# Performance work log

Measured on AMD Instinct MI355X. Metric: run time of the kernel, lower is better.

## Reference

```python
import jax, jax.numpy as jnp
import numpy as np

B, T, D_MODEL, HEADS = 2, 2048, 1024, 16
D_HEAD = D_MODEL // HEADS


def setup_inputs() -> dict:
    key = jax.random.key(0)
    ks = jax.random.split(key, 9)
    s = 1.0 / np.sqrt(D_HEAD)
    return {
        "x": jax.random.normal(ks[0], (B, T, D_MODEL), dtype=jnp.float32),
        "Wq": jax.random.normal(ks[1], (D_HEAD, D_HEAD), dtype=jnp.float32) * s,
        "bq": jax.random.normal(ks[2], (D_HEAD,), dtype=jnp.float32) * 0.01,
        "Wk": jax.random.normal(ks[3], (D_HEAD, D_HEAD), dtype=jnp.float32) * s,
        "bk": jax.random.normal(ks[4], (D_HEAD,), dtype=jnp.float32) * 0.01,
        "Wv": jax.random.normal(ks[5], (D_HEAD, D_HEAD), dtype=jnp.float32) * s,
        "bv": jax.random.normal(ks[6], (D_HEAD,), dtype=jnp.float32) * 0.01,
        "Wp": jax.random.normal(ks[7], (D_MODEL, D_MODEL), dtype=jnp.float32) * (1.0 / np.sqrt(D_MODEL)),
        "bp": jax.random.normal(ks[8], (D_MODEL,), dtype=jnp.float32) * 0.01,
    }


def reference(x, Wq, bq, Wk, bk, Wv, bv, Wp, bp):
    b, t, c = x.shape
    xh = x.reshape(b, t, HEADS, D_HEAD)  # [B,T,H,dh]
    # per-head linear projections (weights shared across heads), nn.Linear: y = x @ W.T + b
    q = jnp.einsum('bthd,ed->bhte', xh, Wq) + bq  # [B,H,T,dh]
    k = jnp.einsum('bthd,ed->bhte', xh, Wk) + bk
    v = jnp.einsum('bthd,ed->bhte', xh, Wv) + bv
    # NOTE: original scales by sqrt(C) = sqrt(d_model), not sqrt(d_head)
    scale = 1.0 / jnp.sqrt(jnp.float32(c))
    att = jnp.einsum('bhqd,bhkd->bhqk', q, k) * scale  # [B,H,T,T]
    att = jax.nn.softmax(att, axis=-1)
    out = jnp.einsum('bhqk,bhkd->bhqd', att, v)  # [B,H,T,dh]
    out = out.transpose(0, 2, 1, 3).reshape(b, t, c)  # [B,T,C]
    out = out @ Wp.T + bp
    return out
```

## Files before the change

### kernel.cpp

```cpp
#include <hip/hip_runtime.h>
#include <hip/hip_bf16.h>

#define B_ 2
#define T_ 2048
#define DM_ 1024
#define H_ 16
#define DH_ 64
#define QSCALE 0.045084220027780106f

typedef unsigned short u16;
typedef unsigned int u32;
typedef __attribute__((ext_vector_type(2))) unsigned int u32x2;
typedef __attribute__((ext_vector_type(4))) unsigned int u32x4;
typedef __attribute__((ext_vector_type(4))) float f32x4v;
typedef __attribute__((ext_vector_type(8))) short bf16x8;
typedef __attribute__((ext_vector_type(4))) float f32x4;
typedef __attribute__((ext_vector_type(16))) float f32x16;

__device__ __forceinline__ u16 f2bf(float f) {
    u32 u = __float_as_uint(f);
    return (u16)((u + 0x7FFF + ((u >> 16) & 1)) >> 16);
}
__device__ __forceinline__ float bf2f(u16 h) {
    return __uint_as_float(((u32)h) << 16);
}
__device__ __forceinline__ float exp2_fast(float x) {
    float r;
    asm("v_exp_f32 %0, %1" : "=v"(r) : "v"(x));
    return r;
}
__device__ __forceinline__ u32 cvtpk_bf16(float lo, float hi) {
    u32 r;
    asm("v_cvt_pk_bf16_f32 %0, %1, %2" : "=v"(r) : "v"(lo), "v"(hi));
    return r;
}

__device__ __forceinline__ const bf16x8* frag_at(const u16* base, int row, int c16) {
    return (const bf16x8*)((const char*)base + row * 128 + ((c16 ^ (row & 7)) << 4));
}

__global__ __launch_bounds__(256) void wsplit_all(
    const float* __restrict__ Wq, const float* __restrict__ Wk,
    const float* __restrict__ Wv, const float* __restrict__ Wp,
    u16* __restrict__ W6, u16* __restrict__ Wh, u16* __restrict__ Wl)
{
    const int i = blockIdx.x * 256 + threadIdx.x;
    if (i < DM_ * DM_) {
        const float w = Wp[i];
        const u16 hi = f2bf(w);
        Wh[i] = hi;
        Wl[i] = f2bf(w - bf2f(hi));
    } else {
        const int j = i - DM_ * DM_;
        const int mat = j >> 12, idx = j & 4095;
        const float w = (mat == 0) ? Wq[idx] : (mat == 1) ? Wk[idx] : Wv[idx];
        const u16 hi = f2bf(w);
        W6[(mat * 2) * 4096 + idx] = hi;
        W6[(mat * 2 + 1) * 4096 + idx] = f2bf(w - bf2f(hi));
    }
}

__global__ __launch_bounds__(256) void qkv_mfma(
    const float* __restrict__ x,
    const float* __restrict__ bq, const float* __restrict__ bk,
    const float* __restrict__ bv, const u16* __restrict__ W6,
    u16* __restrict__ Q, u16* __restrict__ K, u16* __restrict__ VT)
{
    __shared__ u16 Ws[6 * 4096];

    const int tid = threadIdx.x;
    const int wid = tid >> 6;
    const int lane = tid & 63;
    const int li = lane & 15, g = lane >> 4;

    const int bh = blockIdx.x >> 4;
    const int t0 = (blockIdx.x & 15) * 128;
    const int b = bh >> 4, h = bh & 15;
    const int tw0 = t0 + wid * 32;

    #pragma unroll
    for (int j = 0; j < 12; ++j) {
        const int gi = j * 256 + tid;
        const int tile = gi >> 9;
        const int t16 = gi & 511;
        const int r = t16 >> 3, c16 = t16 & 7;
        const int c16s = c16 ^ (r & 7);
        __builtin_amdgcn_global_load_lds(
            (const __attribute__((address_space(1))) u32*)((const char*)W6 + tile * 8192 + r * 128 + (c16s << 4)),
            (__attribute__((address_space(3))) u32*)((char*)Ws + gi * 16),
            16, 0, 0);
    }

    const float* xb = x + ((size_t)b * T_) * DM_ + h * 64;
    f32x4v xr[2][2][2];
    #pragma unroll
    for (int mt = 0; mt < 2; ++mt)
        #pragma unroll
        for (int kt = 0; kt < 2; ++kt) {
            const float* p = xb + (size_t)(tw0 + 16 * mt + li) * DM_ + kt * 32 + g * 8;
            xr[mt][kt][0] = *(const f32x4v*)p;
            xr[mt][kt][1] = *(const f32x4v*)(p + 4);
        }

    float bq_r[4], bk_r[4], bv_r[4][4];
    #pragma unroll
    for (int nt = 0; nt < 4; ++nt) { bq_r[nt] = bq[16 * nt + li]; bk_r[nt] = bk[16 * nt + li]; }
    #pragma unroll
    for (int vd = 0; vd < 4; ++vd)
        #pragma unroll
        for (int rg = 0; rg < 4; ++rg) bv_r[vd][rg] = bv[16 * vd + 4 * g + rg];

    __syncthreads();

    bf16x8 xhf[2][2], xlf[2][2];
    #pragma unroll
    for (int mt = 0; mt < 2; ++mt)
        #pragma unroll
        for (int kt = 0; kt < 2; ++kt) {
            u32 hw[4], lw[4];
            #pragma unroll
            for (int q2 = 0; q2 < 2; ++q2) {
                const f32x4v v = xr[mt][kt][q2];
                const u32 p0 = cvtpk_bf16(v[0], v[1]);
                const u32 p1 = cvtpk_bf16(v[2], v[3]);
                const float l0 = v[0] - __uint_as_float(p0 << 16);
                const float l1 = v[1] - __uint_as_float(p0 & 0xFFFF0000u);
                const float l2 = v[2] - __uint_as_float(p1 << 16);
                const float l3 = v[3] - __uint_as_float(p1 & 0xFFFF0000u);
                hw[q2 * 2] = p0; hw[q2 * 2 + 1] = p1;
                lw[q2 * 2] = cvtpk_bf16(l0, l1);
                lw[q2 * 2 + 1] = cvtpk_bf16(l2, l3);
            }
            xhf[mt][kt] = *(const bf16x8*)hw;
            xlf[mt][kt] = *(const bf16x8*)lw;
        }

    const u16* Wqh = Ws;
    const u16* Wql = Ws + 4096;
    const u16* Wkh = Ws + 8192;
    const u16* Wkl = Ws + 12288;
    const u16* Wvh = Ws + 16384;
    const u16* Wvl = Ws + 20480;

    const size_t qk_base = ((size_t)bh * T_) * DH_;

    {
        f32x4 acc[2][4];
        #pragma unroll
        for (int mt = 0; mt < 2; ++mt)
            #pragma unroll
            for (int nt = 0; nt < 4; ++nt) acc[mt][nt] = (f32x4){0.f, 0.f, 0.f, 0.f};
        #pragma unroll
        for (int nt = 0; nt < 4; ++nt)
            #pragma unroll
            for (int kt = 0; kt < 2; ++kt) {
                const bf16x8 wh = *frag_at(Wqh, 16 * nt + li, 4 * kt + g);
                const bf16x8 wl = *frag_at(Wql, 16 * nt + li, 4 * kt + g);
                #pragma unroll
                for (int mt = 0; mt < 2; ++mt) {
                    acc[mt][nt] = __builtin_amdgcn_mfma_f32_16x16x32_bf16(xhf[mt][kt], wh, acc[mt][nt], 0, 0, 0);
                    acc[mt][nt] = __builtin_amdgcn_mfma_f32_16x16x32_bf16(xlf[mt][kt], wh, acc[mt][nt], 0, 0, 0);
                    acc[mt][nt] = __builtin_amdgcn_mfma_f32_16x16x32_bf16(xhf[mt][kt], wl, acc[mt][nt], 0, 0, 0);
                }
            }
        #pragma unroll
        for (int mt = 0; mt < 2; ++mt)
            #pragma unroll
            for (int rg = 0; rg < 4; ++rg) {
                const int t = tw0 + 16 * mt + 4 * g + rg;
                #pragma unroll
                for (int nt = 0; nt < 4; ++nt)
                    Q[qk_base + (size_t)t * DH_ + 16 * nt + li] =
                        f2bf((acc[mt][nt][rg] + bq_r[nt]) * QSCALE);
            }
    }

    {
        f32x4 acc[2][4];
        #pragma unroll
        for (int mt = 0; mt < 2; ++mt)
            #pragma unroll
            for (int nt = 0; nt < 4; ++nt) acc[mt][nt] = (f32x4){0.f, 0.f, 0.f, 0.f};
        #pragma unroll
        for (int nt = 0; nt < 4; ++nt)
            #pragma unroll
            for (int kt = 0; kt < 2; ++kt) {
                const bf16x8 wh = *frag_at(Wkh, 16 * nt + li, 4 * kt + g);
                const bf16x8 wl = *frag_at(Wkl, 16 * nt + li, 4 * kt + g);
                #pragma unroll
                for (int mt = 0; mt < 2; ++mt) {
                    acc[mt][nt] = __builtin_amdgcn_mfma_f32_16x16x32_bf16(xhf[mt][kt], wh, acc[mt][nt], 0, 0, 0);
                    acc[mt][nt] = __builtin_amdgcn_mfma_f32_16x16x32_bf16(xlf[mt][kt], wh, acc[mt][nt], 0, 0, 0);
                    acc[mt][nt] = __builtin_amdgcn_mfma_f32_16x16x32_bf16(xhf[mt][kt], wl, acc[mt][nt], 0, 0, 0);
                }
            }
        #pragma unroll
        for (int mt = 0; mt < 2; ++mt)
            #pragma unroll
            for (int rg = 0; rg < 4; ++rg) {
                const int t = tw0 + 16 * mt + 4 * g + rg;
                #pragma unroll
                for (int nt = 0; nt < 4; ++nt)
                    K[qk_base + (size_t)t * DH_ + 16 * nt + li] =
                        f2bf(acc[mt][nt][rg] + bk_r[nt]);
            }
    }

    {
        f32x4 acc[4][2];
        #pragma unroll
        for (int vd = 0; vd < 4; ++vd)
            #pragma unroll
            for (int tc = 0; tc < 2; ++tc) acc[vd][tc] = (f32x4){0.f, 0.f, 0.f, 0.f};
        #pragma unroll
        for (int vd = 0; vd < 4; ++vd)
            #pragma unroll
            for (int kt = 0; kt < 2; ++kt) {
                const bf16x8 ah = *frag_at(Wvh, 16 * vd + li, 4 * kt + g);
                const bf16x8 al = *frag_at(Wvl, 16 * vd + li, 4 * kt + g);
                #pragma unroll
                for (int tc = 0; tc < 2; ++tc) {
                    acc[vd][tc] = __builtin_amdgcn_mfma_f32_16x16x32_bf16(ah, xhf[tc][kt], acc[vd][tc], 0, 0, 0);
                    acc[vd][tc] = __builtin_amdgcn_mfma_f32_16x16x32_bf16(al, xhf[tc][kt], acc[vd][tc], 0, 0, 0);
                    acc[vd][tc] = __builtin_amdgcn_mfma_f32_16x16x32_bf16(ah, xlf[tc][kt], acc[vd][tc], 0, 0, 0);
                }
            }
        u16* VTb = VT + (size_t)bh * DH_ * T_;
        #pragma unroll
        for (int vd = 0; vd < 4; ++vd)
            #pragma unroll
            for (int rg = 0; rg < 4; ++rg) {
                const int d = 16 * vd + 4 * g + rg;
                #pragma unroll
                for (int tc = 0; tc < 2; ++tc)
                    VTb[(size_t)d * T_ + tw0 + 16 * tc + li] =
                        f2bf(acc[vd][tc][rg] + bv_r[vd][rg]);
            }
    }
}

__global__ __launch_bounds__(256) void attn_mfma(
    const u16* __restrict__ Q, const u16* __restrict__ K,
    const u16* __restrict__ VT, u16* __restrict__ Ah, u16* __restrict__ Al)
{
    __shared__ char smem[65536];

    const int tid = threadIdx.x;
    const int wid = tid >> 6;
    const int lane = tid & 63;
    const int l = lane & 31, h = lane >> 5;
    const int flat = blockIdx.x;
    const int bh = (flat & 7) + ((flat >> 7) << 3);
    const int qx = (flat >> 3) & 15;
    const int q0 = qx * 128 + wid * 32;

    const size_t bhoff = (size_t)bh * T_ * DH_;

    bf16x8 qf[4];
    {
        const u16* Qp = Q + bhoff + (size_t)(q0 + l) * DH_ + 8 * h;
        #pragma unroll
        for (int kt = 0; kt < 4; ++kt)
            qf[kt] = *(const bf16x8*)(Qp + 16 * kt);
    }

    f32x16 o0 = {}, o1 = {};
    f32x16 sA, sB, sC, sD;
    float l_part = 0.f;

    const char* ldsR[4];
    #pragma unroll
    for (int j = 0; j < 4; ++j)
        ldsR[j] = smem + l * 128 + ((((2 * j + h) ^ (l & 7))) << 4);

    const int sl_r = lane >> 3;
    const int sl_c = (lane & 7) ^ sl_r;
    const char* kgp = (const char*)(K + bhoff) + (32 * wid + sl_r) * 128 + (sl_c << 4);
    const char* vgp = (const char*)(VT + (size_t)bh * DH_ * T_) + (size_t)(16 * wid + sl_r) * (T_ * 2) + (sl_c << 4);
    const int kdst = 32 * wid * 128 + lane * 16;
    const int vdst = 16 * wid * 128 + lane * 16;

#define STAGE(KB_, VB_)                                                                  \
    {                                                                                    \
        _Pragma("unroll")                                                                \
        for (int j = 0; j < 4; ++j)                                                      \
            __builtin_amdgcn_global_load_lds(                                            \
                (const __attribute__((address_space(1))) u32*)(kgp + j * 1024),          \
                (__attribute__((address_space(3))) u32*)(smem + (KB_) + kdst + j * 1024),\
                16, 0, 0);                                                               \
        __builtin_amdgcn_global_load_lds(                                                \
            (const __attribute__((address_space(1))) u32*)vgp,                           \
            (__attribute__((address_space(3))) u32*)(smem + (VB_) + vdst), 16, 0, 0);    \
        __builtin_amdgcn_global_load_lds(                                                \
            (const __attribute__((address_space(1))) u32*)(vgp + 8 * T_ * 2),            \
            (__attribute__((address_space(3))) u32*)(smem + (VB_) + vdst + 1024), 16, 0, 0); \
        __builtin_amdgcn_global_load_lds(                                                \
            (const __attribute__((address_space(1))) u32*)(vgp + 128),                   \
            (__attribute__((address_space(3))) u32*)(smem + (VB_) + 8192 + vdst), 16, 0, 0); \
        __builtin_amdgcn_global_load_lds(                                                \
            (const __attribute__((address_space(1))) u32*)(vgp + 8 * T_ * 2 + 128),      \
            (__attribute__((address_space(3))) u32*)(smem + (VB_) + 8192 + vdst + 1024), 16, 0, 0); \
        kgp += 16384; vgp += 256;                                                        \
    }

#define QK(KB_, S, c)                                                                    \
    {                                                                                    \
        S = (f32x16){};                                                                  \
        _Pragma("unroll")                                                                \
        for (int kt = 0; kt < 4; ++kt) {                                                 \
            const bf16x8 kf = *(const bf16x8*)(ldsR[kt] + (KB_) + (c) * 4096);           \
            S = __builtin_amdgcn_mfma_f32_32x32x16_bf16(kf, qf[kt], S, 0, 0, 0);         \
        }                                                                                \
    }

#define SMPV(S, c, VB_)                                                                  \
    {                                                                                    \
        float lacc = 0.f;                                                                \
        _Pragma("unroll")                                                                \
        for (int r = 0; r < 16; ++r) { S[r] = exp2_fast(S[r]); lacc += S[r]; }           \
        l_part += lacc;                                                                  \
        __builtin_amdgcn_s_setprio(1);                                                   \
        _Pragma("unroll")                                                                \
        for (int ktl = 0; ktl < 2; ++ktl) {                                              \
            const int rb = ktl * 8;                                                      \
            u32 w0 = cvtpk_bf16(S[rb + 0], S[rb + 1]);                                   \
            u32 w1 = cvtpk_bf16(S[rb + 2], S[rb + 3]);                                   \
            u32 w2 = cvtpk_bf16(S[rb + 4], S[rb + 5]);                                   \
            u32 w3 = cvtpk_bf16(S[rb + 6], S[rb + 7]);                                   \
            asm("v_permlane32_swap_b32 %0, %1" : "+v"(w0), "+v"(w2));                    \
            asm("v_permlane32_swap_b32 %0, %1" : "+v"(w1), "+v"(w3));                    \
            u32x4 pw; pw[0] = w0; pw[1] = w1; pw[2] = w2; pw[3] = w3;                    \
            const bf16x8 pf = __builtin_bit_cast(bf16x8, pw);                            \
            const char* vb = ldsR[2 * ((c) & 1) + ktl] + (VB_) + ((c) >> 1) * 8192;      \
            const bf16x8 vf0 = *(const bf16x8*)vb;                                       \
            const bf16x8 vf1 = *(const bf16x8*)(vb + 4096);                              \
            o0 = __builtin_amdgcn_mfma_f32_32x32x16_bf16(vf0, pf, o0, 0, 0, 0);          \
            o1 = __builtin_amdgcn_mfma_f32_32x32x16_bf16(vf1, pf, o1, 0, 0, 0);          \
        }                                                                                \
        __builtin_amdgcn_s_setprio(0);                                                   \
    }

#define ATTN_ITER(KB_, VB_, PKB_, PVB_, DO_PREF)                                         \
    {                                                                                    \
        __syncthreads();                                                                 \
        if (DO_PREF) STAGE(PKB_, PVB_);                                                  \
        __builtin_amdgcn_s_setprio(1);                                                   \
        QK(KB_, sA, 0); QK(KB_, sB, 1); QK(KB_, sC, 2); QK(KB_, sD, 3);                  \
        __builtin_amdgcn_s_setprio(0);                                                   \
        SMPV(sA, 0, VB_); SMPV(sB, 1, VB_); SMPV(sC, 2, VB_); SMPV(sD, 3, VB_);          \
    }

    STAGE(0, 32768);
    for (int it = 0; it < 16; it += 2) {
        ATTN_ITER(0, 32768, 16384, 49152, true);
        ATTN_ITER(16384, 49152, 0, 32768, (it + 2 < 16));
    }
#undef ATTN_ITER
#undef SMPV
#undef QK
#undef STAGE

    const float lt = l_part + __shfl_xor(l_part, 32);
    const float inv = 1.0f / lt;

    __syncthreads();

    char* ehi = smem + wid * 8192;
    char* elo = ehi + 4096;
    #pragma unroll
    for (int db = 0; db < 2; ++db) {
        #pragma unroll
        for (int rr = 0; rr < 4; ++rr) {
            float v0, v1, v2, v3;
            if (db == 0) {
                v0 = o0[4 * rr + 0] * inv; v1 = o0[4 * rr + 1] * inv;
                v2 = o0[4 * rr + 2] * inv; v3 = o0[4 * rr + 3] * inv;
            } else {
                v0 = o1[4 * rr + 0] * inv; v1 = o1[4 * rr + 1] * inv;
                v2 = o1[4 * rr + 2] * inv; v3 = o1[4 * rr + 3] * inv;
            }
            u32x2 wh, wl;
            wh.x = cvtpk_bf16(v0, v1);
            wh.y = cvtpk_bf16(v2, v3);
            const float r0 = v0 - __uint_as_float(wh.x << 16);
            const float r1 = v1 - __uint_as_float(wh.x & 0xFFFF0000u);
            const float r2 = v2 - __uint_as_float(wh.y << 16);
            const float r3 = v3 - __uint_as_float(wh.y & 0xFFFF0000u);
            wl.x = cvtpk_bf16(r0, r1);
            wl.y = cvtpk_bf16(r2, r3);
            const int byteoff = l * 128 + (((4 * db + rr) ^ (l & 7)) << 4) + 8 * h;
            *(u32x2*)(ehi + byteoff) = wh;
            *(u32x2*)(elo + byteoff) = wl;
        }
    }

    const int b = bh >> 4, head = bh & 15;
    const int sub = lane & 7;
    const int row8 = lane >> 3;
    #pragma unroll
    for (int rr = 0; rr < 4; ++rr) {
        const int row = 8 * rr + row8;
        const int byteoff = row * 128 + ((sub ^ row8) << 4);
        const size_t gidx = ((size_t)b * T_ + q0 + row) * DM_ + head * 64 + sub * 8;
        *(u32x4*)(Ah + gidx) = *(const u32x4*)(ehi + byteoff);
        *(u32x4*)(Al + gidx) = *(const u32x4*)(elo + byteoff);
    }
}

__global__ __launch_bounds__(512) void proj_mfma(
    const u16* __restrict__ Ah, const u16* __restrict__ Al,
    const u16* __restrict__ Wh, const u16* __restrict__ Wl,
    const float* __restrict__ bp, float* __restrict__ out)
{
    __shared__ char smem[131072];

    const int tid = threadIdx.x;
    const int wid = tid >> 6;
    const int lane = tid & 63;
    const int li = lane & 15, g = lane >> 4;
    const int row0 = blockIdx.y * 128, col0 = blockIdx.x * 128;

    const int mat = wid >> 1, half = wid & 1;
    const char* gsrc;
    if (mat == 0)      gsrc = (const char*)(Ah + (size_t)row0 * DM_);
    else if (mat == 1) gsrc = (const char*)(Al + (size_t)row0 * DM_);
    else if (mat == 2) gsrc = (const char*)(Wh + (size_t)col0 * DM_);
    else               gsrc = (const char*)(Wl + (size_t)col0 * DM_);
    const int r_local = half * 64 + (lane >> 3);
    const int c16s = (lane & 7) ^ (lane >> 3);
    const char* gp0 = gsrc + (size_t)r_local * (DM_ * 2) + (c16s << 4);
    const int ldst0 = mat * 16384 + half * 8192;

#define PSTAGE(BUF, STEP)                                                                \
    {                                                                                    \
        _Pragma("unroll")                                                                \
        for (int j = 0; j < 8; ++j) {                                                    \
            __builtin_amdgcn_global_load_lds(                                            \
                (const __attribute__((address_space(1))) u32*)(gp0 + (size_t)(STEP) * 128 + (size_t)j * (8 * DM_ * 2)), \
                (__attribute__((address_space(3))) u32*)(smem + (BUF) + ldst0 + j * 1024),\
                16, 0, 0);                                                               \
        }                                                                                \
    }

    const int wr = wid >> 1, wc = wid & 1;

    f32x4 acc[2][4];
    #pragma unroll
    for (int m = 0; m < 2; ++m)
        #pragma unroll
        for (int n = 0; n < 4; ++n) acc[m][n] = (f32x4){0.f, 0.f, 0.f, 0.f};

    PSTAGE(0, 0);
    for (int step = 0; step < 16; ++step) {
        const int buf = (step & 1) * 65536;
        __syncthreads();
        if (step < 15) PSTAGE(buf ^ 65536, step + 1);

        const u16* pAh = (const u16*)(smem + buf);
        const u16* pAl = (const u16*)(smem + buf + 16384);
        const u16* pWh = (const u16*)(smem + buf + 32768);
        const u16* pWl = (const u16*)(smem + buf + 49152);

        __builtin_amdgcn_s_setprio(1);
        #pragma unroll
        for (int kt = 0; kt < 2; ++kt) {
            bf16x8 ah[2], al[2], wh[4], wl[4];
            #pragma unroll
            for (int m = 0; m < 2; ++m) {
                ah[m] = *frag_at(pAh, wr * 32 + m * 16 + li, kt * 4 + g);
                al[m] = *frag_at(pAl, wr * 32 + m * 16 + li, kt * 4 + g);
            }
            #pragma unroll
            for (int n = 0; n < 4; ++n) {
                wh[n] = *frag_at(pWh, wc * 64 + n * 16 + li, kt * 4 + g);
                wl[n] = *frag_at(pWl, wc * 64 + n * 16 + li, kt * 4 + g);
            }
            #pragma unroll
            for (int m = 0; m < 2; ++m)
                #pragma unroll
                for (int n = 0; n < 4; ++n) {
                    acc[m][n] = __builtin_amdgcn_mfma_f32_16x16x32_bf16(ah[m], wh[n], acc[m][n], 0, 0, 0);
                    acc[m][n] = __builtin_amdgcn_mfma_f32_16x16x32_bf16(al[m], wh[n], acc[m][n], 0, 0, 0);
                    acc[m][n] = __builtin_amdgcn_mfma_f32_16x16x32_bf16(ah[m], wl[n], acc[m][n], 0, 0, 0);
                }
        }
        __builtin_amdgcn_s_setprio(0);
    }
#undef PSTAGE

    const int orow = row0 + wr * 32;
    const int ocol = col0 + wc * 64;
    float bias[4];
    #pragma unroll
    for (int n = 0; n < 4; ++n) bias[n] = bp[ocol + n * 16 + li];
    #pragma unroll
    for (int m = 0; m < 2; ++m)
        #pragma unroll
        for (int n = 0; n < 4; ++n)
            #pragma unroll
            for (int q = 0; q < 4; ++q)
                out[(size_t)(orow + m * 16 + g * 4 + q) * DM_ + ocol + n * 16 + li] =
                    acc[m][n][q] + bias[n];
}

extern "C" void kernel_launch(void* const* d_in, const int* in_sizes, int n_in,
                              void* d_out, int out_size, void* d_ws, size_t ws_size,
                              hipStream_t stream) {
    const float* x  = (const float*)d_in[0];
    const float* Wq = (const float*)d_in[1];
    const float* bq = (const float*)d_in[2];
    const float* Wk = (const float*)d_in[3];
    const float* bk = (const float*)d_in[4];
    const float* Wv = (const float*)d_in[5];
    const float* bv = (const float*)d_in[6];
    const float* Wp = (const float*)d_in[7];
    const float* bp = (const float*)d_in[8];
    float* out = (float*)d_out;

    const size_t n_qkv = (size_t)B_ * H_ * T_ * DH_;
    const size_t n_w   = (size_t)DM_ * DM_;
    u16* Qb  = (u16*)d_ws;
    u16* Kb  = Qb + n_qkv;
    u16* VTb = Kb + n_qkv;
    u16* Ahb = VTb + n_qkv;
    u16* Alb = Ahb + n_qkv;
    u16* Whb = Alb + n_qkv;
    u16* Wlb = Whb + n_w;
    u16* W6b = Wlb + n_w;

    wsplit_all<<<(n_w + 12288) / 256, 256, 0, stream>>>(Wq, Wk, Wv, Wp, W6b, Whb, Wlb);
    qkv_mfma<<<32 * 16, 256, 0, stream>>>(x, bq, bk, bv, W6b, Qb, Kb, VTb);
    attn_mfma<<<512, 256, 0, stream>>>(Qb, Kb, VTb, Ahb, Alb);
    proj_mfma<<<dim3(DM_ / 128, (B_ * T_) / 128), 512, 0, stream>>>(Ahb, Alb, Whb, Wlb, bp, out);
}
```

Baseline: 90.12 us.

## Fold weight splitting into QKV and attention kernels, dropping separate launch

Removes the standalone weight-split kernel. The small Wq/Wk/Wv split now happens inside each qkv_mfma block while it loads into LDS, and the Wp split runs as extra blocks interleaved 8:1 with the attention blocks in attn_mfma. This removes one kernel launch and the serialization before qkv and lets the Wp conversion overlap with attention work. In exchange, every qkv block redundantly converts the small weights from fp32, and the attention grid grows to 4608 blocks.

```diff
diff --git a/kernel.cpp b/kernel.cpp
--- a/kernel.cpp
+++ b/kernel.cpp
@@ -39,31 +39,33 @@
     return (const bf16x8*)((const char*)base + row * 128 + ((c16 ^ (row & 7)) << 4));
 }
 
-__global__ __launch_bounds__(256) void wsplit_all(
-    const float* __restrict__ Wq, const float* __restrict__ Wk,
-    const float* __restrict__ Wv, const float* __restrict__ Wp,
-    u16* __restrict__ W6, u16* __restrict__ Wh, u16* __restrict__ Wl)
-{
-    const int i = blockIdx.x * 256 + threadIdx.x;
-    if (i < DM_ * DM_) {
-        const float w = Wp[i];
-        const u16 hi = f2bf(w);
-        Wh[i] = hi;
-        Wl[i] = f2bf(w - bf2f(hi));
-    } else {
-        const int j = i - DM_ * DM_;
-        const int mat = j >> 12, idx = j & 4095;
-        const float w = (mat == 0) ? Wq[idx] : (mat == 1) ? Wk[idx] : Wv[idx];
-        const u16 hi = f2bf(w);
-        W6[(mat * 2) * 4096 + idx] = hi;
-        W6[(mat * 2 + 1) * 4096 + idx] = f2bf(w - bf2f(hi));
-    }
+__device__ __forceinline__ void split8(const f32x4v a, const f32x4v b,
+                                       u32x4* hi, u32x4* lo) {
+    u32x4 h, l;
+    h[0] = cvtpk_bf16(a[0], a[1]);
+    h[1] = cvtpk_bf16(a[2], a[3]);
+    h[2] = cvtpk_bf16(b[0], b[1]);
+    h[3] = cvtpk_bf16(b[2], b[3]);
+    const float l0 = a[0] - __uint_as_float(h[0] << 16);
+    const float l1 = a[1] - __uint_as_float(h[0] & 0xFFFF0000u);
+    const float l2 = a[2] - __uint_as_float(h[1] << 16);
+    const float l3 = a[3] - __uint_as_float(h[1] & 0xFFFF0000u);
+    const float l4 = b[0] - __uint_as_float(h[2] << 16);
+    const float l5 = b[1] - __uint_as_float(h[2] & 0xFFFF0000u);
+    const float l6 = b[2] - __uint_as_float(h[3] << 16);
+    const float l7 = b[3] - __uint_as_float(h[3] & 0xFFFF0000u);
+    l[0] = cvtpk_bf16(l0, l1);
+    l[1] = cvtpk_bf16(l2, l3);
+    l[2] = cvtpk_bf16(l4, l5);
+    l[3] = cvtpk_bf16(l6, l7);
+    *hi = h; *lo = l;
 }
 
 __global__ __launch_bounds__(256) void qkv_mfma(
     const float* __restrict__ x,
-    const float* __restrict__ bq, const float* __restrict__ bk,
-    const float* __restrict__ bv, const u16* __restrict__ W6,
+    const float* __restrict__ Wq, const float* __restrict__ bq,
+    const float* __restrict__ Wk, const float* __restrict__ bk,
+    const float* __restrict__ Wv, const float* __restrict__ bv,
     u16* __restrict__ Q, u16* __restrict__ K, u16* __restrict__ VT)
 {
     __shared__ u16 Ws[6 * 4096];
@@ -79,16 +81,19 @@
     const int tw0 = t0 + wid * 32;
 
     #pragma unroll
-    for (int j = 0; j < 12; ++j) {
-        const int gi = j * 256 + tid;
-        const int tile = gi >> 9;
-        const int t16 = gi & 511;
-        const int r = t16 >> 3, c16 = t16 & 7;
-        const int c16s = c16 ^ (r & 7);
-        __builtin_amdgcn_global_load_lds(
-            (const __attribute__((address_space(1))) u32*)((const char*)W6 + tile * 8192 + r * 128 + (c16s << 4)),
-            (__attribute__((address_space(3))) u32*)((char*)Ws + gi * 16),
-            16, 0, 0);
+    for (int j = 0; j < 6; ++j) {
+        const int idx = (j & 1) * 256 + tid;
+        const int r = idx >> 3, c16 = idx & 7;
+        const float* src = (j < 2) ? Wq : (j < 4) ? Wk : Wv;
+        const float* p = src + r * 64 + c16 * 8;
+        const f32x4v a = *(const f32x4v*)p;
+        const f32x4v bb = *(const f32x4v*)(p + 4);
+        u32x4 hv, lv;
+        split8(a, bb, &hv, &lv);
+        const int dst = r * 128 + ((c16 ^ (r & 7)) << 4);
+        const int mat = j >> 1;
+        *(u32x4*)((char*)Ws + (2 * mat) * 8192 + dst) = hv;
+        *(u32x4*)((char*)Ws + (2 * mat + 1) * 8192 + dst) = lv;
     }
 
     const float* xb = x + ((size_t)b * T_) * DM_ + h * 64;
@@ -117,22 +122,10 @@
     for (int mt = 0; mt < 2; ++mt)
         #pragma unroll
         for (int kt = 0; kt < 2; ++kt) {
-            u32 hw[4], lw[4];
-            #pragma unroll
-            for (int q2 = 0; q2 < 2; ++q2) {
-                const f32x4v v = xr[mt][kt][q2];
-                const u32 p0 = cvtpk_bf16(v[0], v[1]);
-                const u32 p1 = cvtpk_bf16(v[2], v[3]);
-                const float l0 = v[0] - __uint_as_float(p0 << 16);
-                const float l1 = v[1] - __uint_as_float(p0 & 0xFFFF0000u);
-                const float l2 = v[2] - __uint_as_float(p1 << 16);
-                const float l3 = v[3] - __uint_as_float(p1 & 0xFFFF0000u);
-                hw[q2 * 2] = p0; hw[q2 * 2 + 1] = p1;
-                lw[q2 * 2] = cvtpk_bf16(l0, l1);
-                lw[q2 * 2 + 1] = cvtpk_bf16(l2, l3);
-            }
-            xhf[mt][kt] = *(const bf16x8*)hw;
-            xlf[mt][kt] = *(const bf16x8*)lw;
+            u32x4 hv, lv;
+            split8(xr[mt][kt][0], xr[mt][kt][1], &hv, &lv);
+            xhf[mt][kt] = __builtin_bit_cast(bf16x8, hv);
+            xlf[mt][kt] = __builtin_bit_cast(bf16x8, lv);
         }
 
     const u16* Wqh = Ws;
@@ -241,17 +234,31 @@
 
 __global__ __launch_bounds__(256) void attn_mfma(
     const u16* __restrict__ Q, const u16* __restrict__ K,
-    const u16* __restrict__ VT, u16* __restrict__ Ah, u16* __restrict__ Al)
+    const u16* __restrict__ VT, u16* __restrict__ Ah, u16* __restrict__ Al,
+    const float* __restrict__ Wp, u16* __restrict__ Wh, u16* __restrict__ Wl)
 {
     __shared__ char smem[65536];
 
+    const int flat = blockIdx.x;
+    const int m9 = flat % 9;
     const int tid = threadIdx.x;
+
+    if (m9 != 0) {
+        const int wsb = flat - (flat / 9) - 1;
+        const int i = wsb * 256 + tid;
+        const float w = Wp[i];
+        const u16 hi = f2bf(w);
+        Wh[i] = hi;
+        Wl[i] = f2bf(w - bf2f(hi));
+        return;
+    }
+
+    const int aid = flat / 9;
     const int wid = tid >> 6;
     const int lane = tid & 63;
     const int l = lane & 31, h = lane >> 5;
-    const int flat = blockIdx.x;
-    const int bh = (flat & 7) + ((flat >> 7) << 3);
-    const int qx = (flat >> 3) & 15;
+    const int bh = (aid & 7) + ((aid >> 7) << 3);
+    const int qx = (aid >> 3) & 15;
     const int q0 = qx * 128 + wid * 32;
 
     const size_t bhoff = (size_t)bh * T_ * DH_;
@@ -418,7 +425,8 @@
     const int wid = tid >> 6;
     const int lane = tid & 63;
     const int li = lane & 15, g = lane >> 4;
-    const int row0 = blockIdx.y * 128, col0 = blockIdx.x * 128;
+    const int flat = blockIdx.x;
+    const int row0 = (flat >> 3) * 128, col0 = (flat & 7) * 128;
 
     const int mat = wid >> 1, half = wid & 1;
     const char* gsrc;
@@ -526,10 +534,8 @@
     u16* Alb = Ahb + n_qkv;
     u16* Whb = Alb + n_qkv;
     u16* Wlb = Whb + n_w;
-    u16* W6b = Wlb + n_w;
-
-    wsplit_all<<<(n_w + 12288) / 256, 256, 0, stream>>>(Wq, Wk, Wv, Wp, W6b, Whb, Wlb);
-    qkv_mfma<<<32 * 16, 256, 0, stream>>>(x, bq, bk, bv, W6b, Qb, Kb, VTb);
-    attn_mfma<<<512, 256, 0, stream>>>(Qb, Kb, VTb, Ahb, Alb);
-    proj_mfma<<<dim3(DM_ / 128, (B_ * T_) / 128), 512, 0, stream>>>(Ahb, Alb, Whb, Wlb, bp, out);
-}
+
+    qkv_mfma<<<32 * 16, 256, 0, stream>>>(x, Wq, bq, Wk, bk, Wv, bv, Qb, Kb, VTb);
+    attn_mfma<<<4608, 256, 0, stream>>>(Qb, Kb, VTb, Ahb, Alb, Wp, Whb, Wlb);
+    proj_mfma<<<256, 512, 0, stream>>>(Ahb, Alb, Whb, Wlb, bp, out);
+}
```

Result: slower. 104.0 us (+15.4%).
